# Kernel tuning notes

Hardware: AMD Instinct MI355X
Metric: run time of the kernel (lower is better)

Reference implementation:

```python
import jax, jax.numpy as jnp
import numpy as np

EMBED_DIM = 2048
NUM_Q_HEADS = 32
NUM_KV_HEADS = 8
HEAD_DIM = EMBED_DIM // NUM_Q_HEADS
N_REP = NUM_Q_HEADS // NUM_KV_HEADS
B, T = 2, 2048


def setup_inputs() -> dict:
    key = jax.random.key(0)
    ks = jax.random.split(key, 10)
    C = EMBED_DIM
    kv_dim = NUM_KV_HEADS * HEAD_DIM
    s = 1.0 / np.sqrt(C)
    return {
        "x": jax.random.normal(ks[0], (B, T, C), dtype=jnp.float32),
        "mask": jnp.tril(jnp.ones((1, 1, T, T), dtype=bool)),
        "Wq": jax.random.normal(ks[1], (C, C), dtype=jnp.float32) * s,
        "bq": jnp.zeros((C,), dtype=jnp.float32),
        "Wk": jax.random.normal(ks[2], (C, kv_dim), dtype=jnp.float32) * s,
        "bk": jnp.zeros((kv_dim,), dtype=jnp.float32),
        "Wv": jax.random.normal(ks[3], (C, kv_dim), dtype=jnp.float32) * s,
        "bv": jnp.zeros((kv_dim,), dtype=jnp.float32),
        "Wo": jax.random.normal(ks[4], (C, C), dtype=jnp.float32) * s,
        "bo": jnp.zeros((C,), dtype=jnp.float32),
    }


def reference(x, mask, Wq, bq, Wk, bk, Wv, bv, Wo, bo):
    b, t, c = x.shape
    # projections
    q = (x @ Wq + bq).reshape(b, t, NUM_Q_HEADS, HEAD_DIM).transpose(0, 2, 1, 3)   # [B,Hq,T,D]
    k = (x @ Wk + bk).reshape(b, t, NUM_KV_HEADS, HEAD_DIM).transpose(0, 2, 1, 3)  # [B,Hkv,T,D]
    v = (x @ Wv + bv).reshape(b, t, NUM_KV_HEADS, HEAD_DIM).transpose(0, 2, 1, 3)
    # repeat KV heads to match query heads (same math as expand+reshape)
    k = jnp.repeat(k, N_REP, axis=1)  # [B,Hq,T,D]
    v = jnp.repeat(v, N_REP, axis=1)
    scores = jnp.einsum("bhqd,bhkd->bhqk", q, k) / np.sqrt(HEAD_DIM)
    scores = jnp.where(mask, scores, -jnp.inf)
    attn = jax.nn.softmax(scores, axis=-1)
    out = jnp.einsum("bhqk,bhkd->bhqd", attn, v)  # [B,Hq,T,D]
    out = out.transpose(0, 2, 1, 3).reshape(b, t, c)
    return out @ Wo + bo
```

## Files before the change

### kernel.cpp

```cpp
#include <hip/hip_runtime.h>
#include <stdint.h>

typedef __attribute__((ext_vector_type(8))) short bf16x8;
typedef __attribute__((ext_vector_type(4))) float f32x4;

#define LOG2E 1.44269504088896f
#define T_SEQ 2048

__device__ __forceinline__ float bf2f(short s) {
    unsigned u = ((unsigned)(unsigned short)s) << 16;
    float f; __builtin_memcpy(&f, &u, 4); return f;
}
__device__ __forceinline__ short f2bf(float f) {
    unsigned u; __builtin_memcpy(&u, &f, 4);
    u = (u + 0x7FFFu + ((u >> 16) & 1u)) >> 16;
    return (short)u;
}
__device__ __forceinline__ short f2bf_trunc(float f) {
    unsigned u; __builtin_memcpy(&u, &f, 4);
    return (short)(u >> 16);
}

#define GLDS(g, l) __builtin_amdgcn_global_load_lds( \
    (const __attribute__((address_space(1))) void*)(g), \
    (__attribute__((address_space(3))) void*)(l), 16, 0, 0)

__global__ void detect_k(const unsigned short* __restrict__ x, int* __restrict__ flag) {
    int lane = threadIdx.x;
    int cnt = 0;
    for (int i = lane; i < 2048; i += 64) {
        int e = (x[i] >> 7) & 0xFF;
        if (e >= 0xC0) cnt++;
    }
    cnt += __shfl_xor(cnt, 1);
    cnt += __shfl_xor(cnt, 2);
    cnt += __shfl_xor(cnt, 4);
    cnt += __shfl_xor(cnt, 8);
    cnt += __shfl_xor(cnt, 16);
    cnt += __shfl_xor(cnt, 32);
    if (lane == 0) { flag[0] = (cnt >= 32) ? 1 : 0; flag[1] = 0; }
}

__global__ __launch_bounds__(256) void convert_all_k(
    const void* __restrict__ x, short* __restrict__ xb,
    const void* __restrict__ b0, const void* __restrict__ b1,
    const void* __restrict__ b2, const void* __restrict__ b3,
    short* __restrict__ o0, short* __restrict__ o1,
    short* __restrict__ o2, short* __restrict__ o3,
    const int* __restrict__ flag)
{
    const int blk = blockIdx.x;
    const int fp32 = *flag;
    if (blk < 4096) {
        int i = (blk * 256 + threadIdx.x) * 8;
        bf16x8 v;
        if (fp32) {
            const float* f = (const float*)x + i;
            #pragma unroll
            for (int j = 0; j < 8; ++j) v[j] = f2bf(f[j]);
        } else {
            v = *(const bf16x8*)((const short*)x + i);
        }
        *(bf16x8*)(xb + i) = v;
        return;
    }
    int i = ((blk - 4096) * 256 + threadIdx.x) * 8;
    const void* in; short* out; int off;
    if      (i < 2048) { in = b0; out = o0; off = i; }
    else if (i < 2560) { in = b1; out = o1; off = i - 2048; }
    else if (i < 3072) { in = b2; out = o2; off = i - 2560; }
    else if (i < 5120) { in = b3; out = o3; off = i - 3072; }
    else return;
    bf16x8 v;
    if (fp32) {
        const float* f = (const float*)in + off;
        #pragma unroll
        for (int j = 0; j < 8; ++j) v[j] = f2bf(f[j]);
    } else {
        v = *(const bf16x8*)((const short*)in + off);
    }
    *(bf16x8*)(out + off) = v;
}

__global__ __launch_bounds__(256) void transpose_k(
    const void* __restrict__ in_, short* __restrict__ out,
    int R, int ldi, long ibstride, long obstride, const int* __restrict__ flag)
{
    short* ob = out + (long)blockIdx.z * obstride;
    int c = blockIdx.x * 256 + threadIdx.x;
    int r0 = blockIdx.y * 64;
    int fp32 = *flag;
    if (fp32) {
        const float* ib = (const float*)in_ + (long)blockIdx.z * ibstride;
        for (int rr = 0; rr < 64; rr += 8) {
            bf16x8 v;
            #pragma unroll
            for (int j = 0; j < 8; ++j) v[j] = f2bf(ib[(long)(r0 + rr + j) * ldi + c]);
            *(bf16x8*)(ob + (long)c * R + r0 + rr) = v;
        }
    } else {
        const short* ib = (const short*)in_ + (long)blockIdx.z * ibstride;
        for (int rr = 0; rr < 64; rr += 8) {
            bf16x8 v;
            #pragma unroll
            for (int j = 0; j < 8; ++j) v[j] = ib[(long)(r0 + rr + j) * ldi + c];
            *(bf16x8*)(ob + (long)c * R + r0 + rr) = v;
        }
    }
}

__global__ __launch_bounds__(256) void transpose4_k(
    const void* __restrict__ Wq, const void* __restrict__ Wk,
    const void* __restrict__ Wv, const void* __restrict__ Wo,
    short* __restrict__ Wq_t, short* __restrict__ Wkv_t,
    short* __restrict__ Wo_t, const int* __restrict__ flag)
{
    const int bx = blockIdx.x;
    const void* in; short* out; int ldi, c;
    if (bx < 8)       { in = Wq; out = Wq_t;                     ldi = 2048; c = bx * 256 + threadIdx.x; }
    else if (bx < 10) { in = Wk; out = Wkv_t;                    ldi = 512;  c = (bx - 8) * 256 + threadIdx.x; }
    else if (bx < 12) { in = Wv; out = Wkv_t + (long)512 * 2048; ldi = 512;  c = (bx - 10) * 256 + threadIdx.x; }
    else              { in = Wo; out = Wo_t;                     ldi = 2048; c = (bx - 12) * 256 + threadIdx.x; }
    const int r0 = blockIdx.y * 64;
    const int fp32 = *flag;
    if (fp32) {
        const float* ib = (const float*)in;
        for (int rr = 0; rr < 64; rr += 8) {
            bf16x8 v;
            #pragma unroll
            for (int j = 0; j < 8; ++j) v[j] = f2bf(ib[(long)(r0 + rr + j) * ldi + c]);
            *(bf16x8*)(out + (long)c * 2048 + r0 + rr) = v;
        }
    } else {
        const short* ib = (const short*)in;
        for (int rr = 0; rr < 64; rr += 8) {
            bf16x8 v;
            #pragma unroll
            for (int j = 0; j < 8; ++j) v[j] = ib[(long)(r0 + rr + j) * ldi + c];
            *(bf16x8*)(out + (long)c * 2048 + r0 + rr) = v;
        }
    }
}

#define BK 32
template <int BN>
__global__ __launch_bounds__(256) void gemm_bt(
    const short* __restrict__ A, const short* __restrict__ Bt,
    const short* __restrict__ bias1, int nsplit,
    short* __restrict__ C, short* __restrict__ C2, int n2,
    float* __restrict__ Cf, const int* __restrict__ flag,
    int M, int N, int K, int nbx)
{
    constexpr int NT = BN / 32;
    __shared__ short a_lds[128 * BK];
    __shared__ short b_lds[BN * BK];
    const int tid = threadIdx.x;
    const int wave = tid >> 6, lane = tid & 63;
    const int quad = lane >> 4, l16 = lane & 15;

    const int nwg = gridDim.x;
    const int swz = (blockIdx.x & 7) * (nwg >> 3) + (blockIdx.x >> 3);
    const int by = swz / nbx;
    const int bx = swz - by * nbx;
    const int m0 = by * 128, n0 = bx * BN;
    const int wm = (wave >> 1) * 64, wn = (wave & 1) * (BN / 2);

    const int c0i = tid, c1i = 256 + tid;
    const int rA0 = c0i >> 2, kc0 = (c0i & 3) ^ ((rA0 >> 1) & 3);
    const int rA1 = c1i >> 2, kc1 = (c1i & 3) ^ ((rA1 >> 1) & 3);
    const long aoff0 = (long)(m0 + rA0) * K + kc0 * 8;
    const long aoff1 = (long)(m0 + rA1) * K + kc1 * 8;
    const long boff0 = (long)(n0 + rA0) * K + kc0 * 8;
    const long boff1 = (long)(n0 + rA1) * K + kc1 * 8;
    short* alp0 = a_lds + (wave * 64) * 8;
    short* alp1 = a_lds + (256 + wave * 64) * 8;
    short* blp0 = b_lds + (wave * 64) * 8;
    short* blp1 = b_lds + (256 + wave * 64) * 8;

    int aro[4], bro[NT];
    #pragma unroll
    for (int t = 0; t < 4; ++t) {
        int ra = wm + t * 16 + l16;
        aro[t] = ra * BK + (quad ^ ((ra >> 1) & 3)) * 8;
    }
    #pragma unroll
    for (int t = 0; t < NT; ++t) {
        int rb = wn + t * 16 + l16;
        bro[t] = rb * BK + (quad ^ ((rb >> 1) & 3)) * 8;
    }

    f32x4 acc[4][NT];
    #pragma unroll
    for (int i = 0; i < 4; ++i)
        #pragma unroll
        for (int j = 0; j < NT; ++j)
            acc[i][j] = (f32x4){0.f, 0.f, 0.f, 0.f};

    for (int k0 = 0; k0 < K; k0 += BK) {
        __syncthreads();
        GLDS(A + aoff0 + k0, alp0);
        GLDS(A + aoff1 + k0, alp1);
        GLDS(Bt + boff0 + k0, blp0);
        if constexpr (BN == 128) {
            GLDS(Bt + boff1 + k0, blp1);
        } else if constexpr (BN == 96) {
            if (wave < 2) GLDS(Bt + boff1 + k0, blp1);
        }
        __syncthreads();
        bf16x8 af[4], bfr[NT];
        #pragma unroll
        for (int t = 0; t < 4; ++t) af[t] = *(const bf16x8*)(a_lds + aro[t]);
        #pragma unroll
        for (int t = 0; t < NT; ++t) bfr[t] = *(const bf16x8*)(b_lds + bro[t]);
        #pragma unroll
        for (int mt = 0; mt < 4; ++mt)
            #pragma unroll
            for (int nt = 0; nt < NT; ++nt)
                acc[mt][nt] = __builtin_amdgcn_mfma_f32_16x16x32_bf16(
                    af[mt], bfr[nt], acc[mt][nt], 0, 0, 0);
    }

    const int f32o = Cf ? *flag : 0;
    #pragma unroll
    for (int nt = 0; nt < NT; ++nt) {
        int col = n0 + wn + nt * 16 + l16;
        float bb = bf2f(bias1[col < nsplit ? col : 0]);
        #pragma unroll
        for (int mt = 0; mt < 4; ++mt)
            #pragma unroll
            for (int r = 0; r < 4; ++r) {
                int row = m0 + wm + mt * 16 + quad * 4 + r;
                float val = acc[mt][nt][r] + bb;
                if (f32o) {
                    Cf[(long)row * N + col] = val;
                } else if (C2) {
                    if (col < n2) C[(long)row * n2 + col] = f2bf(val);
                    else          C2[(long)row * (N - n2) + (col - n2)] = f2bf(val);
                } else {
                    C[(long)row * N + col] = f2bf(val);
                }
            }
    }
}

#define PLD 68
__global__ __launch_bounds__(256, 4) void attn_k(
    const short* __restrict__ Qf, const short* __restrict__ KVf,
    const short* __restrict__ Vt, short* __restrict__ Attn)
{
    __shared__ short k_lds[64 * PLD];
    __shared__ short vt_lds[64 * PLD];
    __shared__ short p_lds[4 * 32 * PLD];
    const int tid = threadIdx.x;
    const int wave = tid >> 6, lane = tid & 63;
    const int quad = lane >> 4, l16 = lane & 15;

    const int id = blockIdx.x;
    const int bh = id & 63;
    const int w = id >> 6;
    const int QTMAP[16] = {15,13,11,9, 0,2,4,6, 14,12,10,8, 1,3,5,7};
    const int qt = QTMAP[w];
    const int b = bh >> 5, h = bh & 31, hkv = h >> 2;
    const int q0 = qt * 128;
    const int nsteps = 2 * (qt + 1);

    bf16x8 aq[2][2];
    #pragma unroll
    for (int mt = 0; mt < 2; ++mt) {
        const short* qp = Qf + ((long)(b * T_SEQ + q0 + wave * 32 + mt * 16 + l16) * 2048
                                + h * 64 + quad * 8);
        aq[mt][0] = *(const bf16x8*)qp;
        aq[mt][1] = *(const bf16x8*)(qp + 32);
        #pragma unroll
        for (int j = 0; j < 8; ++j) {
            aq[mt][0][j] = f2bf(bf2f(aq[mt][0][j]) * 0.125f);
            aq[mt][1][j] = f2bf(bf2f(aq[mt][1][j]) * 0.125f);
        }
    }

    bf16x8 onesf;
    {
        short o = (l16 == 0) ? (short)0x3F80 : (short)0;
        #pragma unroll
        for (int j = 0; j < 8; ++j) onesf[j] = o;
    }

    f32x4 o_acc[2][4];
    f32x4 l_acc[2];
    #pragma unroll
    for (int mt = 0; mt < 2; ++mt) {
        l_acc[mt] = (f32x4){0.f, 0.f, 0.f, 0.f};
        #pragma unroll
        for (int dt = 0; dt < 4; ++dt) o_acc[mt][dt] = (f32x4){0.f, 0.f, 0.f, 0.f};
    }

    const int cA = tid, cB = 256 + tid;
    const int tA = cA >> 3, chA = cA & 7;
    const int tB = cB >> 3, chB = cB & 7;
    const short* kgA = KVf + ((long)(b * T_SEQ + tA) * 1024 + hkv * 64 + chA * 8);
    const short* kgB = KVf + ((long)(b * T_SEQ + tB) * 1024 + hkv * 64 + chB * 8);
    const short* vgA = Vt + ((long)((b * 8 + hkv) * 64 + tA) * 2048 + chA * 8);
    const short* vgB = Vt + ((long)((b * 8 + hkv) * 64 + tB) * 2048 + chB * 8);

    const int rowq0 = q0 + wave * 32 + quad * 4;
    short* pw = p_lds + (wave * 32 + quad * 4) * PLD + l16;
    const short* pr = p_lds + (wave * 32 + l16) * PLD + quad * 8;

    bf16x8 kA = *(const bf16x8*)(kgA);
    bf16x8 kB = *(const bf16x8*)(kgB);
    bf16x8 vA = *(const bf16x8*)(vgA);
    bf16x8 vB = *(const bf16x8*)(vgB);

    for (int s = 0; s < nsteps; ++s) {
        const int kt0 = s * 64;
        const int ktn = ((s + 1 < nsteps) ? (s + 1) : s) * 64;
        __syncthreads();
        *(bf16x8*)(k_lds + tA * PLD + chA * 8) = kA;
        *(bf16x8*)(k_lds + tB * PLD + chB * 8) = kB;
        *(bf16x8*)(vt_lds + tA * PLD + chA * 8) = vA;
        *(bf16x8*)(vt_lds + tB * PLD + chB * 8) = vB;
        kA = *(const bf16x8*)(kgA + (long)ktn * 1024);
        kB = *(const bf16x8*)(kgB + (long)ktn * 1024);
        vA = *(const bf16x8*)(vgA + ktn);
        vB = *(const bf16x8*)(vgB + ktn);
        __syncthreads();

        const int masked = (kt0 >= q0);
        #pragma unroll
        for (int nt = 0; nt < 4; ++nt) {
            bf16x8 bk0 = *(const bf16x8*)(k_lds + (nt * 16 + l16) * PLD + quad * 8);
            bf16x8 bk1 = *(const bf16x8*)(k_lds + (nt * 16 + l16) * PLD + 32 + quad * 8);
            #pragma unroll
            for (int mt = 0; mt < 2; ++mt) {
                f32x4 z = (f32x4){0.f, 0.f, 0.f, 0.f};
                z = __builtin_amdgcn_mfma_f32_16x16x32_bf16(aq[mt][0], bk0, z, 0, 0, 0);
                z = __builtin_amdgcn_mfma_f32_16x16x32_bf16(aq[mt][1], bk1, z, 0, 0, 0);
                if (!masked) {
                    #pragma unroll
                    for (int r = 0; r < 4; ++r)
                        z[r] = exp2f(fmaf(z[r], LOG2E, -16.0f));
                } else {
                    const int rowq = rowq0 + mt * 16;
                    const int tcol = kt0 + nt * 16 + l16;
                    #pragma unroll
                    for (int r = 0; r < 4; ++r) {
                        float e = exp2f(fmaf(z[r], LOG2E, -16.0f));
                        z[r] = (tcol <= rowq + r) ? e : 0.0f;
                    }
                }
                #pragma unroll
                for (int r = 0; r < 4; ++r)
                    pw[mt * 16 * PLD + r * PLD + nt * 16] = f2bf_trunc(z[r]);
            }
        }

        bf16x8 ap[2][2];
        #pragma unroll
        for (int mt = 0; mt < 2; ++mt) {
            ap[mt][0] = *(const bf16x8*)(pr + mt * 16 * PLD);
            ap[mt][1] = *(const bf16x8*)(pr + mt * 16 * PLD + 32);
        }
        #pragma unroll
        for (int dt = 0; dt < 4; ++dt) {
            bf16x8 bv0 = *(const bf16x8*)(vt_lds + (dt * 16 + l16) * PLD + quad * 8);
            bf16x8 bv1 = *(const bf16x8*)(vt_lds + (dt * 16 + l16) * PLD + 32 + quad * 8);
            #pragma unroll
            for (int mt = 0; mt < 2; ++mt) {
                o_acc[mt][dt] = __builtin_amdgcn_mfma_f32_16x16x32_bf16(ap[mt][0], bv0, o_acc[mt][dt], 0, 0, 0);
                o_acc[mt][dt] = __builtin_amdgcn_mfma_f32_16x16x32_bf16(ap[mt][1], bv1, o_acc[mt][dt], 0, 0, 0);
            }
        }
        #pragma unroll
        for (int mt = 0; mt < 2; ++mt) {
            l_acc[mt] = __builtin_amdgcn_mfma_f32_16x16x32_bf16(ap[mt][0], onesf, l_acc[mt], 0, 0, 0);
            l_acc[mt] = __builtin_amdgcn_mfma_f32_16x16x32_bf16(ap[mt][1], onesf, l_acc[mt], 0, 0, 0);
        }
    }

    #pragma unroll
    for (int mt = 0; mt < 2; ++mt)
        #pragma unroll
        for (int r = 0; r < 4; ++r) {
            const float linv = 1.0f / __shfl(l_acc[mt][r], quad << 4);
            const int rowo = q0 + wave * 32 + mt * 16 + quad * 4 + r;
            short* ap = Attn + (long)(b * T_SEQ + rowo) * 2048 + h * 64 + l16;
            #pragma unroll
            for (int dt = 0; dt < 4; ++dt)
                ap[dt * 16] = f2bf(o_acc[mt][dt][r] * linv);
        }
}

extern "C" void kernel_launch(void* const* d_in, const int* in_sizes, int n_in,
                              void* d_out, int out_size, void* d_ws, size_t ws_size,
                              hipStream_t stream) {
    const void* x  = d_in[0];
    const void* Wq = d_in[2];
    const void* bq = d_in[3];
    const void* Wk = d_in[4];
    const void* bk = d_in[5];
    const void* Wv = d_in[6];
    const void* bv = d_in[7];
    const void* Wo = d_in[8];
    const void* bo = d_in[9];

    short* ws    = (short*)d_ws;
    int*   flags = (int*)ws;
    short* base  = ws + 16;
    short* xb    = base;
    short* Wq_t  = xb + (long)8388608;
    short* Wkv_t = Wq_t + (long)4194304;
    short* regB  = base + (long)17039360;
    short* bqb   = regB;
    short* bkb   = bqb + 2048;
    short* bvb   = bkb + 512;
    short* bob   = bvb + 512;
    short* Wo_t  = bob + 2048;
    short* Qf    = Wo_t + (long)4194304;
    short* KVf   = Qf + (long)8388608;
    short* Vtp   = KVf + (long)4194304;
    short* Attn  = Vtp + (long)2097152;

    detect_k<<<1, 64, 0, stream>>>((const unsigned short*)x, flags);

    convert_all_k<<<4099, 256, 0, stream>>>(x, xb, bq, bk, bv, bo,
                                            bqb, bkb, bvb, bob, flags);

    transpose4_k<<<dim3(20, 32), 256, 0, stream>>>(Wq, Wk, Wv, Wo,
                                                   Wq_t, Wkv_t, Wo_t, flags);

    gemm_bt<96><<<1024, 256, 0, stream>>>(xb, Wq_t, bqb, 3072,
                                          Qf, KVf, 2048, nullptr, flags,
                                          4096, 3072, 2048, 32);

    transpose_k<<<dim3(2, 32, 2), 256, 0, stream>>>(KVf + 512, Vtp, 2048, 1024,
                                                    (long)2048 * 1024, (long)512 * 2048, flags + 1);

    attn_k<<<1024, 256, 0, stream>>>(Qf, KVf, Vtp, Attn);

    gemm_bt<64><<<1024, 256, 0, stream>>>(Attn, Wo_t, bob, 2048,
                                          (short*)d_out, nullptr, 0,
                                          (float*)d_out, flags,
                                          4096, 2048, 2048, 32);
}
```

Baseline: 462.1 us.

## Use 128x128 tiles with BK=64 in projection GEMMs

Rewrites the GEMM to use a uniform 128x128 output tile and doubles the K-step to 64, with a new 8-way XOR LDS swizzle and two MFMA sub-steps per K iteration. This halves the number of barrier-separated load/compute iterations and raises arithmetic intensity per tile. Grids shrink to 768 and 512 workgroups. Risks: higher LDS use (32KB) and more registers reduce occupancy, and fewer workgroups may underfill the 256 CUs.

```diff
diff --git a/kernel.cpp b/kernel.cpp
--- a/kernel.cpp
+++ b/kernel.cpp
@@ -142,18 +142,16 @@
     }
 }
 
-#define BK 32
-template <int BN>
-__global__ __launch_bounds__(256) void gemm_bt(
+#define BK 64
+__global__ __launch_bounds__(256, 3) void gemm_bt(
     const short* __restrict__ A, const short* __restrict__ Bt,
     const short* __restrict__ bias1, int nsplit,
     short* __restrict__ C, short* __restrict__ C2, int n2,
     float* __restrict__ Cf, const int* __restrict__ flag,
     int M, int N, int K, int nbx)
 {
-    constexpr int NT = BN / 32;
     __shared__ short a_lds[128 * BK];
-    __shared__ short b_lds[BN * BK];
+    __shared__ short b_lds[128 * BK];
     const int tid = threadIdx.x;
     const int wave = tid >> 6, lane = tid & 63;
     const int quad = lane >> 4, l16 = lane & 15;
@@ -162,67 +160,66 @@
     const int swz = (blockIdx.x & 7) * (nwg >> 3) + (blockIdx.x >> 3);
     const int by = swz / nbx;
     const int bx = swz - by * nbx;
-    const int m0 = by * 128, n0 = bx * BN;
-    const int wm = (wave >> 1) * 64, wn = (wave & 1) * (BN / 2);
-
-    const int c0i = tid, c1i = 256 + tid;
-    const int rA0 = c0i >> 2, kc0 = (c0i & 3) ^ ((rA0 >> 1) & 3);
-    const int rA1 = c1i >> 2, kc1 = (c1i & 3) ^ ((rA1 >> 1) & 3);
-    const long aoff0 = (long)(m0 + rA0) * K + kc0 * 8;
-    const long aoff1 = (long)(m0 + rA1) * K + kc1 * 8;
-    const long boff0 = (long)(n0 + rA0) * K + kc0 * 8;
-    const long boff1 = (long)(n0 + rA1) * K + kc1 * 8;
-    short* alp0 = a_lds + (wave * 64) * 8;
-    short* alp1 = a_lds + (256 + wave * 64) * 8;
-    short* blp0 = b_lds + (wave * 64) * 8;
-    short* blp1 = b_lds + (256 + wave * 64) * 8;
-
-    int aro[4], bro[NT];
+    const int m0 = by * 128, n0 = bx * 128;
+    const int wm = (wave >> 1) * 64, wn = (wave & 1) * 64;
+
+    long aoff[4], boff[4];
+    #pragma unroll
+    for (int g = 0; g < 4; ++g) {
+        const int c = g * 256 + tid;
+        const int row = c >> 3;
+        const int kc = (c & 7) ^ (row & 7);
+        aoff[g] = (long)(m0 + row) * K + kc * 8;
+        boff[g] = (long)(n0 + row) * K + kc * 8;
+    }
+
+    int aro[4][2], bro[4][2];
     #pragma unroll
     for (int t = 0; t < 4; ++t) {
-        int ra = wm + t * 16 + l16;
-        aro[t] = ra * BK + (quad ^ ((ra >> 1) & 3)) * 8;
-    }
-    #pragma unroll
-    for (int t = 0; t < NT; ++t) {
-        int rb = wn + t * 16 + l16;
-        bro[t] = rb * BK + (quad ^ ((rb >> 1) & 3)) * 8;
-    }
-
-    f32x4 acc[4][NT];
+        const int ra = wm + t * 16 + l16;
+        const int rb = wn + t * 16 + l16;
+        #pragma unroll
+        for (int h = 0; h < 2; ++h) {
+            aro[t][h] = ra * BK + (((h << 2) + quad) ^ (ra & 7)) * 8;
+            bro[t][h] = rb * BK + (((h << 2) + quad) ^ (rb & 7)) * 8;
+        }
+    }
+
+    f32x4 acc[4][4];
     #pragma unroll
     for (int i = 0; i < 4; ++i)
         #pragma unroll
-        for (int j = 0; j < NT; ++j)
+        for (int j = 0; j < 4; ++j)
             acc[i][j] = (f32x4){0.f, 0.f, 0.f, 0.f};
 
     for (int k0 = 0; k0 < K; k0 += BK) {
         __syncthreads();
-        GLDS(A + aoff0 + k0, alp0);
-        GLDS(A + aoff1 + k0, alp1);
-        GLDS(Bt + boff0 + k0, blp0);
-        if constexpr (BN == 128) {
-            GLDS(Bt + boff1 + k0, blp1);
-        } else if constexpr (BN == 96) {
-            if (wave < 2) GLDS(Bt + boff1 + k0, blp1);
-        }
+        #pragma unroll
+        for (int g = 0; g < 4; ++g)
+            GLDS(A + aoff[g] + k0, a_lds + (g * 256 + wave * 64) * 8);
+        #pragma unroll
+        for (int g = 0; g < 4; ++g)
+            GLDS(Bt + boff[g] + k0, b_lds + (g * 256 + wave * 64) * 8);
         __syncthreads();
-        bf16x8 af[4], bfr[NT];
-        #pragma unroll
-        for (int t = 0; t < 4; ++t) af[t] = *(const bf16x8*)(a_lds + aro[t]);
-        #pragma unroll
-        for (int t = 0; t < NT; ++t) bfr[t] = *(const bf16x8*)(b_lds + bro[t]);
-        #pragma unroll
-        for (int mt = 0; mt < 4; ++mt)
-            #pragma unroll
-            for (int nt = 0; nt < NT; ++nt)
-                acc[mt][nt] = __builtin_amdgcn_mfma_f32_16x16x32_bf16(
-                    af[mt], bfr[nt], acc[mt][nt], 0, 0, 0);
+        #pragma unroll
+        for (int h = 0; h < 2; ++h) {
+            bf16x8 af[4], bfr[4];
+            #pragma unroll
+            for (int t = 0; t < 4; ++t) af[t] = *(const bf16x8*)(a_lds + aro[t][h]);
+            #pragma unroll
+            for (int t = 0; t < 4; ++t) bfr[t] = *(const bf16x8*)(b_lds + bro[t][h]);
+            #pragma unroll
+            for (int mt = 0; mt < 4; ++mt)
+                #pragma unroll
+                for (int nt = 0; nt < 4; ++nt)
+                    acc[mt][nt] = __builtin_amdgcn_mfma_f32_16x16x32_bf16(
+                        af[mt], bfr[nt], acc[mt][nt], 0, 0, 0);
+        }
     }
 
     const int f32o = Cf ? *flag : 0;
     #pragma unroll
-    for (int nt = 0; nt < NT; ++nt) {
+    for (int nt = 0; nt < 4; ++nt) {
         int col = n0 + wn + nt * 16 + l16;
         float bb = bf2f(bias1[col < nsplit ? col : 0]);
         #pragma unroll
@@ -428,17 +425,17 @@
     transpose4_k<<<dim3(20, 32), 256, 0, stream>>>(Wq, Wk, Wv, Wo,
                                                    Wq_t, Wkv_t, Wo_t, flags);
 
-    gemm_bt<96><<<1024, 256, 0, stream>>>(xb, Wq_t, bqb, 3072,
-                                          Qf, KVf, 2048, nullptr, flags,
-                                          4096, 3072, 2048, 32);
+    gemm_bt<<<768, 256, 0, stream>>>(xb, Wq_t, bqb, 3072,
+                                     Qf, KVf, 2048, nullptr, flags,
+                                     4096, 3072, 2048, 24);
 
     transpose_k<<<dim3(2, 32, 2), 256, 0, stream>>>(KVf + 512, Vtp, 2048, 1024,
                                                     (long)2048 * 1024, (long)512 * 2048, flags + 1);
 
     attn_k<<<1024, 256, 0, stream>>>(Qf, KVf, Vtp, Attn);
 
-    gemm_bt<64><<<1024, 256, 0, stream>>>(Attn, Wo_t, bob, 2048,
-                                          (short*)d_out, nullptr, 0,
-                                          (float*)d_out, flags,
-                                          4096, 2048, 2048, 32);
-}
+    gemm_bt<<<512, 256, 0, stream>>>(Attn, Wo_t, bob, 2048,
+                                     (short*)d_out, nullptr, 0,
+                                     (float*)d_out, flags,
+                                     4096, 2048, 2048, 16);
+}
```

Result: faster. 400.5 us (-13.3%).
